# Kernel tuning notes

Measured on AMD Instinct MI355X. Metric: run time of the kernel, lower is better.

## Reference

```python
import jax, jax.numpy as jnp
import numpy as np
from jax import lax

FILTERS = 32
NEIGH = 5


def _conv3d_same(x, w, b=None):
    out = lax.conv_general_dilated(x, w, window_strides=(1, 1, 1), padding='SAME',
                                   dimension_numbers=('NCDHW', 'OIDHW', 'NCDHW'))
    return out if b is None else out + b[None, :, None, None, None]


def _avgpool2(x):
    s = lax.reduce_window(x, 0.0, lax.add, (1, 1, 2, 2, 2), (1, 1, 2, 2, 2), 'VALID')
    return s * 0.125


def _grid_sample_3d(vol, grid):
    # trilinear, zeros padding, align_corners=False (torch defaults)
    Din, Hin, Win = vol.shape
    ix = ((grid[..., 0] + 1.0) * Win - 1.0) * 0.5
    iy = ((grid[..., 1] + 1.0) * Hin - 1.0) * 0.5
    iz = ((grid[..., 2] + 1.0) * Din - 1.0) * 0.5
    x0f, y0f, z0f = jnp.floor(ix), jnp.floor(iy), jnp.floor(iz)
    wx, wy, wz = ix - x0f, iy - y0f, iz - z0f
    x0 = x0f.astype(jnp.int32); y0 = y0f.astype(jnp.int32); z0 = z0f.astype(jnp.int32)

    def tap(z, y, x, w):
        valid = (z >= 0) & (z < Din) & (y >= 0) & (y < Hin) & (x >= 0) & (x < Win)
        v = vol[jnp.clip(z, 0, Din - 1), jnp.clip(y, 0, Hin - 1), jnp.clip(x, 0, Win - 1)]
        return jnp.where(valid, v, 0.0) * w

    return (tap(z0,     y0,     x0,     (1 - wz) * (1 - wy) * (1 - wx))
          + tap(z0,     y0,     x0 + 1, (1 - wz) * (1 - wy) * wx)
          + tap(z0,     y0 + 1, x0,     (1 - wz) * wy * (1 - wx))
          + tap(z0,     y0 + 1, x0 + 1, (1 - wz) * wy * wx)
          + tap(z0 + 1, y0,     x0,     wz * (1 - wy) * (1 - wx))
          + tap(z0 + 1, y0,     x0 + 1, wz * (1 - wy) * wx)
          + tap(z0 + 1, y0 + 1, x0,     wz * wy * (1 - wx))
          + tap(z0 + 1, y0 + 1, x0 + 1, wz * wy * wx))


def _forward(x, conv_w, conv_b, gaus_w):
    D = _avgpool2(_conv3d_same(x, conv_w, conv_b))           # (B, c, h, w, d)
    p = _conv3d_same(D, gaus_w)                              # (B, c, h, w, d)
    B, c, h, w, d = D.shape
    # normalized coordinate field P: (3, h, w, d)
    P = jnp.stack([
        jnp.broadcast_to(jnp.arange(h, dtype=D.dtype)[:, None, None] / (h - 1), (h, w, d)),
        jnp.broadcast_to(jnp.arange(w, dtype=D.dtype)[None, :, None] / (w - 1), (h, w, d)),
        jnp.broadcast_to(jnp.arange(d, dtype=D.dtype)[None, None, :] / (d - 1), (h, w, d)),
    ])
    # (B, 3, c, h, w, d) -> (3B, c, h, w, d) for a single batched gaussian conv
    D_mul = (P[None, :, None] * D[:, None]).reshape(3 * B, c, h, w, d)
    allf = _conv3d_same(D_mul, gaus_w).reshape(B, 3, c, h, w, d)
    filt = jnp.clip(allf / (p[:, None] + 1e-6) * 2.0 - 1.0, -1.0, 1.0)
    grids = jnp.transpose(filt, (0, 2, 3, 4, 5, 1))          # (B, c, h, w, d, 3)
    Bx, Cx, Hx, Wx, Dx = x.shape
    vols = x.reshape(B * c, Hx, Wx, Dx)
    g = grids.reshape(B * c, h, w, d, 3)
    y = jax.vmap(_grid_sample_3d)(vols, g).reshape(B, c, h, w, d)
    return y, D, jnp.mean(grids, axis=1)


def setup_inputs() -> dict:
    key = jax.random.key(0)
    k1, k2, k3 = jax.random.split(key, 3)
    x = jax.random.normal(k1, (2, FILTERS, 64, 64, 64), dtype=jnp.float32)
    fan_in = FILTERS * 3 * 3 * 3
    conv_w = (jax.random.normal(k2, (FILTERS, FILTERS, 3, 3, 3), dtype=jnp.float32)
              / np.float32(np.sqrt(fan_in)))
    conv_b = jax.random.normal(k3, (FILTERS,), dtype=jnp.float32) * 0.01
    # fixed gaussian kernel, replicated across in/out channels (as in makegaussian)
    center = NEIGH // 2
    co = np.arange(NEIGH) - center
    zz, yy, xx = np.meshgrid(co, co, co, indexing='ij')
    gk = np.exp(-4.0 * np.log(2.0) * (zz ** 2 + yy ** 2 + xx ** 2) / NEIGH ** 2).astype(np.float32)
    gaus_w = jnp.asarray(np.broadcast_to(gk, (FILTERS, FILTERS, NEIGH, NEIGH, NEIGH)).copy())
    return {"x": x, "conv_w": conv_w, "conv_b": conv_b, "gaus_w": gaus_w}


def reference(x, conv_w, conv_b, gaus_w):
    return _forward(x, conv_w, conv_b, gaus_w)
```

## Files before the change

kernel.cpp:

```cpp
#include <hip/hip_runtime.h>
#include <hip/hip_bf16.h>


#define XN 64
#define DN 32
#define C  32
#define XVOL (XN * XN * XN)
#define DVOL (DN * DN * DN)

typedef __attribute__((ext_vector_type(8))) short short8v;
typedef __attribute__((ext_vector_type(4))) float float4v;

struct __attribute__((packed, aligned(4))) f4u { float4v v; };
struct __attribute__((packed, aligned(4))) s8u { short8v v; };

static __device__ __forceinline__ short f2bf(float f) {
    union { float f; unsigned u; } v; v.f = f;
    unsigned r = (v.u + 0x7fffu + ((v.u >> 16) & 1u)) >> 16;
    return (short)r;
}

static __device__ __forceinline__ unsigned pk2(float a, float b) {
    __hip_bfloat162 h = __float22bfloat162_rn(float2{a, b});
    union { __hip_bfloat162 h2; unsigned u; } cv; cv.h2 = h;
    return cv.u;
}

static __device__ __forceinline__ float4v shmask(float4v ld, float c, float l, float r) {
    float4v o;
    o[0] = fmaf(r, ld[1], c * ld[0]);
    o[1] = fmaf(l, ld[0], fmaf(r, ld[2], c * ld[1]));
    o[2] = fmaf(l, ld[1], fmaf(r, ld[3], c * ld[2]));
    o[3] = fmaf(l, ld[2], c * ld[3]);
    return o;
}

static __device__ __forceinline__ float w4val(const float* __restrict__ conv_w,
                                              int ic, int u, int oc) {
    int uz = u >> 4, uy = (u >> 2) & 3, ux = u & 3;
    float s = 0.f;
    #pragma unroll
    for (int sz = 0; sz < 2; ++sz) {
        int tz = uz - sz; if (tz < 0 || tz > 2) continue;
        #pragma unroll
        for (int sy = 0; sy < 2; ++sy) {
            int ty = uy - sy; if (ty < 0 || ty > 2) continue;
            #pragma unroll
            for (int sx = 0; sx < 2; ++sx) {
                int tx = ux - sx; if (tx < 0 || tx > 2) continue;
                s += conv_w[(oc * C + ic) * 27 + tz * 9 + ty * 3 + tx];
            }
        }
    }
    return 0.125f * s;
}

__global__ __launch_bounds__(256) void k_prep(const float* __restrict__ conv_w,
                                              const float* __restrict__ conv_b,
                                              unsigned short* __restrict__ wfrag,
                                              float* __restrict__ wsum) {
    int bid = blockIdx.x;
    int tid = threadIdx.x;
    if (bid < 256) {
        int i = bid * 256 + tid;
        int e = i & 7;
        int l = (i >> 3) & 63;
        int sf = i >> 9;
        int f = sf & 1, step = sf >> 1;
        int oc = f * 16 + (l & 15);
        int k = step * 32 + ((l >> 4) * 8 + e);
        float v = w4val(conv_w, k >> 6, k & 63, oc);
        wfrag[i] = (unsigned short)f2bf(v);
        if (i == 0) {
            float s = 0.f;
            for (int o = 0; o < C; ++o) s += conv_b[o];
            wsum[2048] = s;
        }
    } else {
        int i2 = (bid - 256) * 256 + tid;
        int oc = tid & 31;
        int kk = i2 >> 5;
        float v = w4val(conv_w, kk >> 6, kk & 63, oc);
        v += __shfl_xor(v, 1, 64);
        v += __shfl_xor(v, 2, 64);
        v += __shfl_xor(v, 4, 64);
        v += __shfl_xor(v, 8, 64);
        v += __shfl_xor(v, 16, 64);
        if (oc == 0) wsum[kk] = v;
    }
}

__global__ __launch_bounds__(256) void k_conv_mfma(
        const float* __restrict__ x, const unsigned short* __restrict__ wfrag,
        const float* __restrict__ wsum, const float* __restrict__ bias,
        float* __restrict__ Dout, float* __restrict__ Dsum) {
    __shared__ float wsl[2112];
    __shared__ char wbuf[2 * 8320];
    int tid = threadIdx.x;
    for (int i = tid; i < 513; i += 256)
        *(float4v*)&wsl[i * 4] = *(const float4v*)&wsum[i * 4];

    int bid = blockIdx.x;
    int wid = (bid & 7) * 128 + (bid >> 3);
    int xt = wid & 1;
    int yt = (wid >> 1) & 15;
    int zt = (wid >> 5) & 15;
    int b  = wid >> 9;
    int w = tid >> 6, lane = tid & 63;
    int col = lane & 15, g = lane >> 4;
    int pz = zt * 2 + (w >> 1), py = yt * 2 + (w & 1), px = xt * 16 + col;

    const char* xb = (const char*)(x + (size_t)b * C * XVOL);
    const char* wfb = (const char*)wfrag;

    int sdst = (tid >> 6) * 1040 + (tid & 63) * 16;

    int gxb = 2 * px - 1;
    int gxc = min(max(gxb, 0), XN - 4);
    int s = gxc - gxb;
    int offb[4];
    float mc[4], ml[4], mr[4];
    #pragma unroll
    for (int h = 0; h < 2; ++h)
    #pragma unroll
    for (int rs = 0; rs < 2; ++rs) {
        int gz = 2 * pz - 1 + 2 * h + (g >> 1);
        int gy = 2 * py - 1 + (g & 1) * 2 + rs;
        bool rv = (unsigned)gz < (unsigned)XN && (unsigned)gy < (unsigned)XN;
        int gzc = min(max(gz, 0), XN - 1);
        int gyc = min(max(gy, 0), XN - 1);
        int idx = h * 2 + rs;
        offb[idx] = ((gzc * XN + gyc) * XN + gxc) * 4;
        mc[idx] = (rv && s == 0)  ? 1.f : 0.f;
        ml[idx] = (rv && s == 1)  ? 1.f : 0.f;
        mr[idx] = (rv && s == -1) ? 1.f : 0.f;
    }

    float4v acc0 = {0.f, 0.f, 0.f, 0.f};
    float4v acc1 = {0.f, 0.f, 0.f, 0.f};
    float dp = 0.f;
    float4v tA[4], tB[4];
    short8v sg0, sg1;

#define LOADT(T, j) do {                                                     \
    const char* xp = xb + (size_t)(j) * (XVOL * 4);                          \
    _Pragma("unroll")                                                        \
    for (int i5 = 0; i5 < 4; ++i5)                                           \
        T[i5] = ((const f4u*)(xp + offb[i5]))->v;                            \
} while (0)

#define STAGE_LOAD(st) do {                                                  \
    const char* wp = wfb + (size_t)(st) * 8192 + tid * 16;                   \
    sg0 = ((const s8u*)(wp))->v;                                             \
    sg1 = ((const s8u*)(wp + 4096))->v;                                      \
} while (0)

#define STAGE_WRITE(bf) do {                                                 \
    *(short8v*)(wbuf + (bf) * 8320 + sdst) = sg0;                            \
    *(short8v*)(wbuf + (bf) * 8320 + 4160 + sdst) = sg1;                     \
} while (0)

#define COMPT(T, bf, icL, j) do {                                            \
    _Pragma("unroll")                                                        \
    for (int h5 = 0; h5 < 2; ++h5) {                                         \
        float4v r0 = shmask(T[h5 * 2],     mc[h5 * 2],     ml[h5 * 2],     mr[h5 * 2]);     \
        float4v r1 = shmask(T[h5 * 2 + 1], mc[h5 * 2 + 1], ml[h5 * 2 + 1], mr[h5 * 2 + 1]); \
        const float4v wlo = *(const float4v*)&wsl[((j) * 2 + h5) * 32 + g * 8];     \
        const float4v whi = *(const float4v*)&wsl[((j) * 2 + h5) * 32 + g * 8 + 4]; \
        dp = fmaf(wlo[0], r0[0], dp); dp = fmaf(wlo[1], r0[1], dp);          \
        dp = fmaf(wlo[2], r0[2], dp); dp = fmaf(wlo[3], r0[3], dp);          \
        dp = fmaf(whi[0], r1[0], dp); dp = fmaf(whi[1], r1[1], dp);          \
        dp = fmaf(whi[2], r1[2], dp); dp = fmaf(whi[3], r1[3], dp);          \
        union { short8v s; unsigned u[4]; } Bv;                              \
        Bv.u[0] = pk2(r0[0], r0[1]); Bv.u[1] = pk2(r0[2], r0[3]);            \
        Bv.u[2] = pk2(r1[0], r1[1]); Bv.u[3] = pk2(r1[2], r1[3]);            \
        const char* wl = wbuf + (bf) * 8320 + (icL) * 4160 + lane * 16;      \
        short8v w0 = *(const short8v*)(wl + (h5 * 2) * 1040);                \
        short8v w1 = *(const short8v*)(wl + (h5 * 2 + 1) * 1040);            \
        acc0 = __builtin_amdgcn_mfma_f32_16x16x32_bf16(w0, Bv.s, acc0, 0, 0, 0); \
        acc1 = __builtin_amdgcn_mfma_f32_16x16x32_bf16(w1, Bv.s, acc1, 0, 0, 0); \
    }                                                                        \
} while (0)

    STAGE_LOAD(0);
    STAGE_WRITE(0);
    LOADT(tA, 0);
    LOADT(tB, 1);
    __syncthreads();

    for (int st = 0; st < 16; ++st) {
        int cur = st & 1;
        if (st < 15) STAGE_LOAD(st + 1);
        int ic = st * 2;
        COMPT(tA, cur, 0, ic);
        if (ic + 2 < C) LOADT(tA, ic + 2);
        COMPT(tB, cur, 1, ic + 1);
        if (ic + 3 < C) LOADT(tB, ic + 3);
        if (st < 15) {
            STAGE_WRITE(cur ^ 1);
            __syncthreads();
        }
    }

#undef LOADT
#undef STAGE_LOAD
#undef STAGE_WRITE
#undef COMPT

    dp += __shfl_xor(dp, 16, 64);
    dp += __shfl_xor(dp, 32, 64);

    int sp = pz * (DN * DN) + py * DN + px;
    float4v b0 = *(const float4v*)&bias[g * 4];
    float4v b1 = *(const float4v*)&bias[16 + g * 4];
    #pragma unroll
    for (int r = 0; r < 4; ++r) {
        int oc0 = g * 4 + r;
        int oc1 = 16 + g * 4 + r;
        Dout[(size_t)(b * C + oc0) * DVOL + sp] = acc0[r] + b0[r];
        Dout[(size_t)(b * C + oc1) * DVOL + sp] = acc1[r] + b1[r];
    }
    if (g == 0)
        Dsum[b * DVOL + sp] = dp + wsl[2048];
}

__global__ __launch_bounds__(256) void k_gauss(const float* __restrict__ Dsum,
                                               const float* __restrict__ gaus_w,
                                               float* __restrict__ filt,
                                               float* __restrict__ outg) {
    __shared__ float tg[8 * 12 * 12];
    __shared__ float gk[125];
    int bid = blockIdx.x;
    int xt = bid & 3, yt = (bid >> 2) & 3, zt = (bid >> 4) & 7, b = bid >> 7;
    int tid = threadIdx.x;
    if (tid < 125) gk[tid] = gaus_w[tid];
    const float* Ds = Dsum + b * DVOL;
    for (int i = tid; i < 1152; i += 256) {
        int lx = i % 12; int r = i / 12; int ly = r % 12; int lz = r / 12;
        int gz = zt * 4 - 2 + lz, gy = yt * 8 - 2 + ly, gx = xt * 8 - 2 + lx;
        float v = 0.f;
        if ((unsigned)gz < DN && (unsigned)gy < DN && (unsigned)gx < DN)
            v = Ds[(gz * DN + gy) * DN + gx];
        tg[i] = v;
    }
    __syncthreads();
    int px = tid & 7, py = (tid >> 3) & 7, pz = tid >> 6;
    const float inv31 = 1.f / 31.f;
    float zb = (float)(zt * 4 + pz - 2);
    float yb = (float)(yt * 8 + py - 2);
    float xb = (float)(xt * 8 + px - 2);
    float p = 0.f, a0 = 0.f, a1 = 0.f, a2 = 0.f;
    for (int tz = 0; tz < 5; ++tz)
    for (int ty = 0; ty < 5; ++ty) {
        int base = ((pz + tz) * 12 + py + ty) * 12 + px;
        #pragma unroll
        for (int tx = 0; tx < 5; ++tx) {
            float g = gk[tz * 25 + ty * 5 + tx];
            float v = g * tg[base + tx];
            p += v;
            a0 = fmaf(v, (zb + (float)tz) * inv31, a0);
            a1 = fmaf(v, (yb + (float)ty) * inv31, a1);
            a2 = fmaf(v, (xb + (float)tx) * inv31, a2);
        }
    }
    float denom = p + 1e-6f;
    float f0 = fminf(fmaxf(a0 / denom * 2.f - 1.f, -1.f), 1.f);
    float f1 = fminf(fmaxf(a1 / denom * 2.f - 1.f, -1.f), 1.f);
    float f2 = fminf(fmaxf(a2 / denom * 2.f - 1.f, -1.f), 1.f);
    int sp = ((zt * 4 + pz) * DN + yt * 8 + py) * DN + xt * 8 + px;
    filt[(b * 3 + 0) * DVOL + sp] = f0;
    filt[(b * 3 + 1) * DVOL + sp] = f1;
    filt[(b * 3 + 2) * DVOL + sp] = f2;
    outg[(size_t)(b * DVOL + sp) * 3 + 0] = f0;
    outg[(size_t)(b * DVOL + sp) * 3 + 1] = f1;
    outg[(size_t)(b * DVOL + sp) * 3 + 2] = f2;
}

__global__ __launch_bounds__(128) void k_sample(const float* __restrict__ x,
                                                const float* __restrict__ filt,
                                                float* __restrict__ y) {
    int bid = blockIdx.x;
    int wid = (bid & 7) * 1024 + (bid >> 3);
    int xt = wid & 1;
    int yt = (wid >> 1) & 7;
    int zt = (wid >> 4) & 15;
    int cgrp = (wid >> 8) & 15;
    int b  = wid >> 12;
    int tid = threadIdx.x;
    int px = tid & 15, py = (tid >> 4) & 3, pz = tid >> 6;
    int sp = ((zt * 2 + pz) * DN + yt * 4 + py) * DN + xt * 16 + px;
    const float* fb = filt + b * 3 * DVOL;
    float g0 = fb[sp], g1 = fb[DVOL + sp], g2 = fb[2 * DVOL + sp];

    float ix = ((g0 + 1.0f) * (float)XN - 1.0f) * 0.5f;
    float iy = ((g1 + 1.0f) * (float)XN - 1.0f) * 0.5f;
    float iz = ((g2 + 1.0f) * (float)XN - 1.0f) * 0.5f;
    float x0f = floorf(ix), y0f = floorf(iy), z0f = floorf(iz);
    float wx = ix - x0f, wyf = iy - y0f, wz = iz - z0f;
    int x0 = (int)x0f, y0i = (int)y0f, z0 = (int)z0f;

    int offs[8];
    float wts[8];
    #pragma unroll
    for (int t = 0; t < 8; ++t) {
        int dz = t >> 2, dy = (t >> 1) & 1, dx = t & 1;
        int zc = z0 + dz, yc = y0i + dy, xc = x0 + dx;
        bool valid = (unsigned)zc < (unsigned)XN && (unsigned)yc < (unsigned)XN &&
                     (unsigned)xc < (unsigned)XN;
        int zcl = min(max(zc, 0), XN - 1);
        int ycl = min(max(yc, 0), XN - 1);
        int xcl = min(max(xc, 0), XN - 1);
        offs[t] = zcl * (XN * XN) + ycl * XN + xcl;
        float w = (dz ? wz : 1.f - wz) * (dy ? wyf : 1.f - wyf) * (dx ? wx : 1.f - wx);
        wts[t] = valid ? w : 0.f;
    }

    const float* xc0 = x + (size_t)(b * C + cgrp * 2) * XVOL;
    float t0[8], t1[8];
    #pragma unroll
    for (int k = 0; k < 8; ++k) t0[k] = xc0[offs[k]];
    #pragma unroll
    for (int k = 0; k < 8; ++k) t1[k] = xc0[XVOL + offs[k]];

    float a0 = 0.f, a1 = 0.f;
    #pragma unroll
    for (int k = 0; k < 8; ++k) a0 = fmaf(wts[k], t0[k], a0);
    #pragma unroll
    for (int k = 0; k < 8; ++k) a1 = fmaf(wts[k], t1[k], a1);
    y[(size_t)(b * C + cgrp * 2 + 0) * DVOL + sp] = a0;
    y[(size_t)(b * C + cgrp * 2 + 1) * DVOL + sp] = a1;
}

extern "C" void kernel_launch(void* const* d_in, const int* in_sizes, int n_in,
                              void* d_out, int out_size, void* d_ws, size_t ws_size,
                              hipStream_t stream) {
    const float* x      = (const float*)d_in[0];
    const float* conv_w = (const float*)d_in[1];
    const float* conv_b = (const float*)d_in[2];
    const float* gaus_w = (const float*)d_in[3];

    float* out = (float*)d_out;
    float* y_out = out;
    float* D_out = out + (size_t)2097152;
    float* g_out = out + (size_t)4194304;

    float* ws   = (float*)d_ws;
    float* Dsum = ws;
    float* filt = ws + 65536;
    float* wsum = ws + 262144;
    unsigned short* wfrag = (unsigned short*)(ws + 264256);

    k_prep<<<dim3(512), dim3(256), 0, stream>>>(conv_w, conv_b, wfrag, wsum);
    k_conv_mfma<<<dim3(1024), dim3(256), 0, stream>>>(x, wfrag, wsum, conv_b,
                                                      D_out, Dsum);
    k_gauss<<<dim3(256), dim3(256), 0, stream>>>(Dsum, gaus_w, filt, g_out);
    k_sample<<<dim3(8192), dim3(128), 0, stream>>>(x, filt, y_out);
    (void)in_sizes; (void)n_in; (void)out_size; (void)ws_size;
}
```

Baseline: 85.00 us.

## Halve conv block to two waves and stage one input channel per step

The fused conv+pool MFMA kernel now uses 128-thread blocks covering one z-row pair of outputs, so twice as many blocks are launched. The weight double-buffer shrinks to one input channel per stage, which means 32 smaller pipeline steps with a barrier each instead of 16. The channel-sum dot product also becomes a vectorized float4 accumulation reduced at the end. The aim is better occupancy and load balance and less LDS per block, at the cost of more barriers and more global weight staging traffic per output.

```diff
diff --git a/kernel.cpp b/kernel.cpp
--- a/kernel.cpp
+++ b/kernel.cpp
@@ -90,30 +90,30 @@
     }
 }
 
-__global__ __launch_bounds__(256) void k_conv_mfma(
+__global__ __launch_bounds__(128) void k_conv_mfma(
         const float* __restrict__ x, const unsigned short* __restrict__ wfrag,
         const float* __restrict__ wsum, const float* __restrict__ bias,
         float* __restrict__ Dout, float* __restrict__ Dsum) {
     __shared__ float wsl[2112];
-    __shared__ char wbuf[2 * 8320];
+    __shared__ char wbuf[2 * 4160];
     int tid = threadIdx.x;
-    for (int i = tid; i < 513; i += 256)
+    for (int i = tid; i < 513; i += 128)
         *(float4v*)&wsl[i * 4] = *(const float4v*)&wsum[i * 4];
 
     int bid = blockIdx.x;
-    int wid = (bid & 7) * 128 + (bid >> 3);
+    int wid = (bid & 7) * 256 + (bid >> 3);
     int xt = wid & 1;
     int yt = (wid >> 1) & 15;
-    int zt = (wid >> 5) & 15;
-    int b  = wid >> 9;
+    int zt = (wid >> 5) & 31;
+    int b  = wid >> 10;
     int w = tid >> 6, lane = tid & 63;
     int col = lane & 15, g = lane >> 4;
-    int pz = zt * 2 + (w >> 1), py = yt * 2 + (w & 1), px = xt * 16 + col;
+    int pz = zt, py = yt * 2 + w, px = xt * 16 + col;
 
     const char* xb = (const char*)(x + (size_t)b * C * XVOL);
     const char* wfb = (const char*)wfrag;
 
-    int sdst = (tid >> 6) * 1040 + (tid & 63) * 16;
+    int sdst = (tid >> 5) * 1040 + (tid & 31) * 32;
 
     int gxb = 2 * px - 1;
     int gxc = min(max(gxb, 0), XN - 4);
@@ -138,7 +138,7 @@
 
     float4v acc0 = {0.f, 0.f, 0.f, 0.f};
     float4v acc1 = {0.f, 0.f, 0.f, 0.f};
-    float dp = 0.f;
+    float4v dpv = {0.f, 0.f, 0.f, 0.f};
     float4v tA[4], tB[4];
     short8v sg0, sg1;
 
@@ -150,31 +150,29 @@
 } while (0)
 
 #define STAGE_LOAD(st) do {                                                  \
-    const char* wp = wfb + (size_t)(st) * 8192 + tid * 16;                   \
+    const char* wp = wfb + (size_t)(st) * 4096 + tid * 32;                   \
     sg0 = ((const s8u*)(wp))->v;                                             \
-    sg1 = ((const s8u*)(wp + 4096))->v;                                      \
+    sg1 = ((const s8u*)(wp + 16))->v;                                        \
 } while (0)
 
 #define STAGE_WRITE(bf) do {                                                 \
-    *(short8v*)(wbuf + (bf) * 8320 + sdst) = sg0;                            \
-    *(short8v*)(wbuf + (bf) * 8320 + 4160 + sdst) = sg1;                     \
+    *(short8v*)(wbuf + (bf) * 4160 + sdst) = sg0;                            \
+    *(short8v*)(wbuf + (bf) * 4160 + sdst + 16) = sg1;                       \
 } while (0)
 
-#define COMPT(T, bf, icL, j) do {                                            \
+#define COMPT(T, bf, j) do {                                                 \
     _Pragma("unroll")                                                        \
     for (int h5 = 0; h5 < 2; ++h5) {                                         \
         float4v r0 = shmask(T[h5 * 2],     mc[h5 * 2],     ml[h5 * 2],     mr[h5 * 2]);     \
         float4v r1 = shmask(T[h5 * 2 + 1], mc[h5 * 2 + 1], ml[h5 * 2 + 1], mr[h5 * 2 + 1]); \
         const float4v wlo = *(const float4v*)&wsl[((j) * 2 + h5) * 32 + g * 8];     \
         const float4v whi = *(const float4v*)&wsl[((j) * 2 + h5) * 32 + g * 8 + 4]; \
-        dp = fmaf(wlo[0], r0[0], dp); dp = fmaf(wlo[1], r0[1], dp);          \
-        dp = fmaf(wlo[2], r0[2], dp); dp = fmaf(wlo[3], r0[3], dp);          \
-        dp = fmaf(whi[0], r1[0], dp); dp = fmaf(whi[1], r1[1], dp);          \
-        dp = fmaf(whi[2], r1[2], dp); dp = fmaf(whi[3], r1[3], dp);          \
+        dpv += wlo * r0;                                                     \
+        dpv += whi * r1;                                                     \
         union { short8v s; unsigned u[4]; } Bv;                              \
         Bv.u[0] = pk2(r0[0], r0[1]); Bv.u[1] = pk2(r0[2], r0[3]);            \
         Bv.u[2] = pk2(r1[0], r1[1]); Bv.u[3] = pk2(r1[2], r1[3]);            \
-        const char* wl = wbuf + (bf) * 8320 + (icL) * 4160 + lane * 16;      \
+        const char* wl = wbuf + (bf) * 4160 + lane * 16;                     \
         short8v w0 = *(const short8v*)(wl + (h5 * 2) * 1040);                \
         short8v w1 = *(const short8v*)(wl + (h5 * 2 + 1) * 1040);            \
         acc0 = __builtin_amdgcn_mfma_f32_16x16x32_bf16(w0, Bv.s, acc0, 0, 0, 0); \
@@ -188,15 +186,17 @@
     LOADT(tB, 1);
     __syncthreads();
 
-    for (int st = 0; st < 16; ++st) {
+    for (int st = 0; st < C; ++st) {
         int cur = st & 1;
-        if (st < 15) STAGE_LOAD(st + 1);
-        int ic = st * 2;
-        COMPT(tA, cur, 0, ic);
-        if (ic + 2 < C) LOADT(tA, ic + 2);
-        COMPT(tB, cur, 1, ic + 1);
-        if (ic + 3 < C) LOADT(tB, ic + 3);
-        if (st < 15) {
+        if (st < C - 1) STAGE_LOAD(st + 1);
+        if (cur == 0) {
+            COMPT(tA, cur, st);
+            if (st + 2 < C) LOADT(tA, st + 2);
+        } else {
+            COMPT(tB, cur, st);
+            if (st + 2 < C) LOADT(tB, st + 2);
+        }
+        if (st < C - 1) {
             STAGE_WRITE(cur ^ 1);
             __syncthreads();
         }
@@ -207,6 +207,7 @@
 #undef STAGE_WRITE
 #undef COMPT
 
+    float dp = (dpv[0] + dpv[1]) + (dpv[2] + dpv[3]);
     dp += __shfl_xor(dp, 16, 64);
     dp += __shfl_xor(dp, 32, 64);
 
@@ -351,7 +352,7 @@
     unsigned short* wfrag = (unsigned short*)(ws + 264256);
 
     k_prep<<<dim3(512), dim3(256), 0, stream>>>(conv_w, conv_b, wfrag, wsum);
-    k_conv_mfma<<<dim3(1024), dim3(256), 0, stream>>>(x, wfrag, wsum, conv_b,
+    k_conv_mfma<<<dim3(2048), dim3(128), 0, stream>>>(x, wfrag, wsum, conv_b,
                                                       D_out, Dsum);
     k_gauss<<<dim3(256), dim3(256), 0, stream>>>(Dsum, gaus_w, filt, g_out);
     k_sample<<<dim3(8192), dim3(128), 0, stream>>>(x, filt, y_out);
```

Measured after the change: 104.2 us. 22.6% more time.
